# Kernel tuning notes

Measured on AMD Instinct MI355X. Metric: run time of the kernel, lower is better.

The kernel has to match this reference:

```python
import jax, jax.numpy as jnp
import numpy as np

TOPK = 8
NUM_SEM = 32


def _forward(x, sem_w, sem_b, q_w, k_w, v_w, fuse_w, fuse_b, alpha, ln_gamma, ln_beta):
    B, C, H, W = x.shape
    N = H * W
    xf = x.reshape(B, C, N)

    # semantic soft-assignment (softmax over K regions per position)
    sem_logits = jnp.einsum('kc,bcn->bkn', sem_w, xf) + sem_b[None, :, None]
    sem = jax.nn.softmax(sem_logits, axis=1)
    sem = jnp.nan_to_num(sem, posinf=1e-6, neginf=0.0)

    # 1x1 conv projections as GEMMs
    q = jnp.einsum('dc,bcn->bdn', q_w, xf)   # (B,d,N)
    k = jnp.einsum('dc,bcn->bdn', k_w, xf)   # (B,d,N)
    v = jnp.einsum('oc,bcn->bon', v_w, xf)   # (B,C,N)
    d = q.shape[1]
    scale = d ** 0.5 + 1e-6

    # --- dense semantic-region attention branch ---
    region_k = jnp.einsum('bkn,bdn->bkd', sem, k)
    region_v = jnp.einsum('bkn,bcn->bkc', sem, v)
    attn_region = jax.nn.softmax(jnp.einsum('bdn,bkd->bkn', q, region_k) / scale, axis=1)
    attn_region = jnp.nan_to_num(attn_region, posinf=1e6, neginf=-1e6)
    cont_out = jnp.einsum('bkn,bkc->bcn', attn_region, region_v)
    cont_out = jnp.nan_to_num(cont_out, posinf=1e6, neginf=-1e6)

    # --- sparse top-k gather attention branch ---
    M = min(256, N)
    _, ti = jax.lax.top_k(jax.lax.stop_gradient(sem), M)       # (B,K,M) top positions per region
    hr = jnp.argmax(sem, axis=1)                                # (B,N) hard region per position
    idx_pp = jnp.take_along_axis(ti, hr[:, :, None], axis=1)    # (B,N,M) pool indices for each position

    bidx = jnp.arange(B)[:, None, None]
    qt = jnp.swapaxes(q, 1, 2)  # (B,N,d)
    kt = jnp.swapaxes(k, 1, 2)  # (B,N,d)
    vt = jnp.swapaxes(v, 1, 2)  # (B,N,C)

    kg = kt[bidx, idx_pp]                                       # (B,N,M,d) gathered key pool
    sims = jnp.einsum('bnd,bnmd->bnm', qt, kg) / scale          # (B,N,M)
    kn = min(TOPK, M)
    topv, topi = jax.lax.top_k(sims, kn)                        # (B,N,kn)
    att = jax.nn.softmax(topv, axis=-1)
    actual = jnp.take_along_axis(idx_pp, topi, axis=2)          # (B,N,kn) spatial indices
    vg = vt[bidx, actual]                                       # (B,N,kn,C)
    sparse_out = jnp.swapaxes(jnp.einsum('bnt,bntc->bnc', att, vg), 1, 2)  # (B,C,N)
    sparse_out = jnp.nan_to_num(sparse_out, posinf=1e6, neginf=-1e6)

    # --- combine, fuse, residual, channel LayerNorm ---
    a = jax.nn.sigmoid(alpha)
    combined = a * cont_out + (1.0 - a) * sparse_out
    combined = jnp.nan_to_num(combined, posinf=1e6, neginf=-1e6)
    fused = jnp.einsum('oc,bcn->bon', fuse_w, combined) + fuse_b[None, :, None]
    out = x + fused.reshape(B, C, H, W)

    xp = out.transpose(0, 2, 3, 1)  # (B,H,W,C)
    mu = xp.mean(-1, keepdims=True)
    var = xp.var(-1, keepdims=True)
    xp = (xp - mu) / jnp.sqrt(var + 1e-5) * ln_gamma + ln_beta
    return xp.transpose(0, 3, 1, 2)


def setup_inputs() -> dict:
    key = jax.random.key(0)
    ks = jax.random.split(key, 8)
    B, C, H, W = 2, 256, 64, 64
    d = C // 4  # reduction=4
    Ksem = NUM_SEM
    f32 = jnp.float32
    return {
        'x': jax.random.normal(ks[0], (B, C, H, W), f32),
        'sem_w': jax.random.normal(ks[1], (Ksem, C), f32) * 0.05,
        'sem_b': jnp.zeros((Ksem,), f32),
        'q_w': jax.random.normal(ks[2], (d, C), f32) * (2.0 / C) ** 0.5,
        'k_w': jax.random.normal(ks[3], (d, C), f32) * (2.0 / C) ** 0.5,
        'v_w': jax.random.normal(ks[4], (C, C), f32) * (2.0 / C) ** 0.5,
        'fuse_w': jax.random.normal(ks[5], (C, C), f32) * (1.0 / C) ** 0.5,
        'fuse_b': jnp.zeros((C,), f32),
        'alpha': jnp.float32(0.5),
        'ln_gamma': jnp.ones((C,), f32),
        'ln_beta': jnp.zeros((C,), f32),
    }


def reference(x, sem_w, sem_b, q_w, k_w, v_w, fuse_w, fuse_b, alpha, ln_gamma, ln_beta):
    return _forward(x, sem_w, sem_b, q_w, k_w, v_w, fuse_w, fuse_b, alpha, ln_gamma, ln_beta)
```

## Files before the change

### kernel.cpp

```cpp
#include <hip/hip_runtime.h>
#include <math.h>

#define QOFF 32
#define KOFF 96
#define VOFF 160
#define NSUB 8

__global__ __launch_bounds__(256) void proj_kernel(
    const float* __restrict__ x,
    const float* __restrict__ sem_w, const float* __restrict__ sem_b,
    const float* __restrict__ q_w, const float* __restrict__ k_w,
    const float* __restrict__ v_w, float* __restrict__ Y)
{
    const int t = threadIdx.x;
    const int n0 = blockIdx.x * 64;
    const int oc0 = blockIdx.y * 64;
    const int b = blockIdx.z;
    const int ty = t >> 4, tx = t & 15;

    __shared__ float As[16][68];
    __shared__ float Bs[16][64];

    float acc[4][4];
#pragma unroll
    for (int i = 0; i < 4; i++)
#pragma unroll
        for (int j = 0; j < 4; j++) acc[i][j] = 0.f;

    const int oc_l = t >> 2;
    const int cp = t & 3;
    const int oc_g = oc0 + oc_l;
    const float* wrow = nullptr;
    if (oc_g < 32) wrow = sem_w + oc_g * 256;
    else if (oc_g < 96) wrow = q_w + (oc_g - 32) * 256;
    else if (oc_g < 160) wrow = k_w + (oc_g - 96) * 256;
    else if (oc_g < 416) wrow = v_w + (oc_g - 160) * 256;

    const int bk = t >> 4;
    const int bn = (t & 15) << 2;

    for (int c0 = 0; c0 < 256; c0 += 16) {
        __syncthreads();
        float4 w4 = make_float4(0.f, 0.f, 0.f, 0.f);
        if (wrow) w4 = *(const float4*)(wrow + c0 + (cp << 2));
        As[(cp << 2) + 0][oc_l] = w4.x;
        As[(cp << 2) + 1][oc_l] = w4.y;
        As[(cp << 2) + 2][oc_l] = w4.z;
        As[(cp << 2) + 3][oc_l] = w4.w;
        *(float4*)&Bs[bk][bn] =
            *(const float4*)(x + ((size_t)(b * 256 + c0 + bk)) * 4096 + n0 + bn);
        __syncthreads();
#pragma unroll
        for (int kk = 0; kk < 16; kk++) {
            float4 a4 = *(float4*)&As[kk][ty << 2];
            float4 b4 = *(float4*)&Bs[kk][tx << 2];
            acc[0][0] += a4.x * b4.x; acc[0][1] += a4.x * b4.y;
            acc[0][2] += a4.x * b4.z; acc[0][3] += a4.x * b4.w;
            acc[1][0] += a4.y * b4.x; acc[1][1] += a4.y * b4.y;
            acc[1][2] += a4.y * b4.z; acc[1][3] += a4.y * b4.w;
            acc[2][0] += a4.z * b4.x; acc[2][1] += a4.z * b4.y;
            acc[2][2] += a4.z * b4.z; acc[2][3] += a4.z * b4.w;
            acc[3][0] += a4.w * b4.x; acc[3][1] += a4.w * b4.y;
            acc[3][2] += a4.w * b4.z; acc[3][3] += a4.w * b4.w;
        }
    }

    if (oc0 + (ty << 2) < 416) {
        float bias[4];
#pragma unroll
        for (int i = 0; i < 4; i++) {
            int oc = oc0 + (ty << 2) + i;
            bias[i] = (oc < 32) ? sem_b[oc] : 0.f;
        }
#pragma unroll
        for (int j = 0; j < 4; j++) {
            int n = n0 + (tx << 2) + j;
            float4 o4 = make_float4(acc[0][j] + bias[0], acc[1][j] + bias[1],
                                    acc[2][j] + bias[2], acc[3][j] + bias[3]);
            *(float4*)(Y + ((size_t)(b * 4096 + n)) * 416 + oc0 + (ty << 2)) = o4;
        }
    }
}

__global__ __launch_bounds__(256) void semsoft_kernel(float* __restrict__ Y,
                                                      int* __restrict__ hr)
{
    const int g = blockIdx.x * 256 + threadIdx.x;
    float* row = Y + (size_t)g * 416;
    float v[32];
#pragma unroll
    for (int i = 0; i < 8; i++) *(float4*)&v[i * 4] = *(float4*)&row[i * 4];
    float mx = v[0]; int am = 0;
#pragma unroll
    for (int kk = 1; kk < 32; kk++) if (v[kk] > mx) { mx = v[kk]; am = kk; }
    float s = 0.f;
#pragma unroll
    for (int kk = 0; kk < 32; kk++) { v[kk] = expf(v[kk] - mx); s += v[kk]; }
    const float inv = 1.f / s;
#pragma unroll
    for (int kk = 0; kk < 32; kk++) v[kk] *= inv;
#pragma unroll
    for (int i = 0; i < 8; i++) *(float4*)&row[i * 4] = *(float4*)&v[i * 4];
    hr[g] = am;
}

__global__ __launch_bounds__(256) void bin_kernel(
    const int* __restrict__ hr, int* __restrict__ cnt, int* __restrict__ plist)
{
    const int g = blockIdx.x * 256 + threadIdx.x;
    const int b = g >> 12, n = g & 4095;
    const int r = hr[g];
    const int slot = atomicAdd(&cnt[b * 32 + r], 1);
    plist[((size_t)(b * 32 + r)) * 4096 + slot] = n;
}

__global__ __launch_bounds__(256) void region_partial_kernel(
    const float* __restrict__ Y, float* __restrict__ P)
{
    const int ch = blockIdx.x;
    const int b  = blockIdx.y;
    const int dg = blockIdx.z;
    const int t = threadIdx.x;
    __shared__ float sem_s[16][33];
    __shared__ float kv_s[16][68];
    const int kg = t >> 4;
    const int dq = t & 15;
    float acc[2][4];
#pragma unroll
    for (int i = 0; i < 2; i++)
#pragma unroll
        for (int j = 0; j < 4; j++) acc[i][j] = 0.f;

    const size_t gbase = (size_t)(b * 4096 + ch * 128);
    const int sr = t >> 4, sc = (t & 15) << 2;
    for (int r0 = 0; r0 < 128; r0 += 16) {
        __syncthreads();
        {
            sem_s[t >> 5][t & 31] = Y[(gbase + r0 + (t >> 5)) * 416 + (t & 31)];
            const int i2 = t + 256;
            sem_s[i2 >> 5][i2 & 31] = Y[(gbase + r0 + (i2 >> 5)) * 416 + (i2 & 31)];
        }
        {
            *(float4*)&kv_s[sr][sc] =
                *(const float4*)(Y + (gbase + r0 + sr) * 416 + 96 + dg * 64 + sc);
        }
        __syncthreads();
#pragma unroll
        for (int r = 0; r < 16; r++) {
            const float s0 = sem_s[r][(kg << 1) + 0];
            const float s1 = sem_s[r][(kg << 1) + 1];
            const float4 kv = *(float4*)&kv_s[r][dq << 2];
            acc[0][0] += s0 * kv.x; acc[0][1] += s0 * kv.y;
            acc[0][2] += s0 * kv.z; acc[0][3] += s0 * kv.w;
            acc[1][0] += s1 * kv.x; acc[1][1] += s1 * kv.y;
            acc[1][2] += s1 * kv.z; acc[1][3] += s1 * kv.w;
        }
    }
    float* Pb = P + ((size_t)(b * 32 + ch)) * 10240 + dg * 64;
#pragma unroll
    for (int i = 0; i < 2; i++)
        *(float4*)&Pb[((kg << 1) + i) * 320 + (dq << 2)] =
            make_float4(acc[i][0], acc[i][1], acc[i][2], acc[i][3]);
}

__global__ __launch_bounds__(256) void region_reduce_kernel(
    const float* __restrict__ P, float* __restrict__ region)
{
    const int idx = blockIdx.x * 256 + threadIdx.x;
    if (idx >= 2 * 10240) return;
    const int b = idx / 10240, rem = idx - b * 10240;
    float s = 0.f;
    for (int ch = 0; ch < 32; ch++)
        s += P[((size_t)(b * 32 + ch)) * 10240 + rem];
    region[(size_t)b * 10240 + rem] = s;
}

__global__ __launch_bounds__(256) void topk_sem_kernel(
    const float* __restrict__ Y, int* __restrict__ ti)
{
    const int kreg = blockIdx.x, b = blockIdx.y;
    const int t = threadIdx.x;
    __shared__ int wpart[4];
    __shared__ int sh_eq[256];
    __shared__ int ctr;

    unsigned int uv[16];
    const int nbase = t * 16;
#pragma unroll
    for (int i = 0; i < 16; i++) {
        float v = Y[((size_t)(b * 4096 + nbase + i)) * 416 + kreg];
        unsigned int u = __float_as_uint(v);
        uv[i] = (u & 0x80000000u) ? ~u : (u | 0x80000000u);
    }
    unsigned long long lo = 0ull, hi = 0xFFFFFFFFull;
    while (lo < hi) {
        const unsigned int mid = (unsigned int)((lo + hi + 1ull) >> 1);
        int c = 0;
#pragma unroll
        for (int i = 0; i < 16; i++) c += (uv[i] >= mid) ? 1 : 0;
#pragma unroll
        for (int off = 1; off < 64; off <<= 1) c += __shfl_xor(c, off);
        __syncthreads();
        if ((t & 63) == 0) wpart[t >> 6] = c;
        __syncthreads();
        const int tot = wpart[0] + wpart[1] + wpart[2] + wpart[3];
        if (tot >= 256) lo = mid; else hi = (unsigned long long)mid - 1ull;
    }
    const unsigned int T = (unsigned int)lo;
    int cgt = 0, ceq = 0;
#pragma unroll
    for (int i = 0; i < 16; i++) { cgt += (uv[i] > T) ? 1 : 0; ceq += (uv[i] == T) ? 1 : 0; }
    int cg = cgt;
#pragma unroll
    for (int off = 1; off < 64; off <<= 1) cg += __shfl_xor(cg, off);
    __syncthreads();
    if ((t & 63) == 0) wpart[t >> 6] = cg;
    sh_eq[t] = ceq;
    if (t == 0) ctr = 0;
    __syncthreads();
    const int c1 = wpart[0] + wpart[1] + wpart[2] + wpart[3];
    int eqbase = 0;
    for (int i = 0; i < t; i++) eqbase += sh_eq[i];
    int* outp = ti + ((size_t)(b * 32 + kreg)) * 256;
    int seen = 0;
#pragma unroll
    for (int i = 0; i < 16; i++) {
        if (uv[i] > T) {
            int pos = atomicAdd(&ctr, 1);
            outp[pos] = nbase + i;
        } else if (uv[i] == T) {
            int r = eqbase + seen; seen++;
            if (c1 + r < 256) outp[c1 + r] = nbase + i;
        }
    }
}

__global__ __launch_bounds__(256) void sparse_attn_kernel(
    const float* __restrict__ Y, const int* __restrict__ cnt,
    const int* __restrict__ plist, const int* __restrict__ ti,
    float* __restrict__ sp)
{
    const int rb = blockIdx.x;
    const int sub = blockIdx.y;
    const int b = rb >> 5;
    const int t = threadIdx.x, wid = t >> 6, lane = t & 63;

    int count = cnt[rb];
    count = min(max(count, 0), 4096);
    const int chunk = (count + NSUB - 1) / NSUB;
    const int p0 = sub * chunk;
    const int p1 = min(p0 + chunk, count);
    if (p1 <= p0) return;
    const int npass = (p1 - p0 + 15) >> 4;

    __shared__ int pool_s[256];
    __shared__ float K_sT[64][256];
    __shared__ float q_sT[4][64][4];

    if (t < 64)
        *(int4*)&pool_s[t << 2] = *(const int4*)(ti + (size_t)rb * 256 + (t << 2));
    __syncthreads();
    {
        const int krow = t >> 1, jh = t & 1;
#pragma unroll
        for (int hh = 0; hh < 2; hh++) {
            const int key = (hh << 7) + krow;
            const int kidx = pool_s[key];
            const float* kr = Y + ((size_t)((b << 12) + kidx)) * 416 + KOFF + (jh << 5);
#pragma unroll
            for (int jj = 0; jj < 8; jj++) {
                float4 kv = *(const float4*)(kr + (jj << 2));
                const int jb = (jh << 5) + (jj << 2);
                K_sT[jb + 0][key] = kv.x;
                K_sT[jb + 1][key] = kv.y;
                K_sT[jb + 2][key] = kv.z;
                K_sT[jb + 3][key] = kv.w;
            }
        }
    }
    __syncthreads();

    const float inv_scale = 1.0f / (8.0f + 1e-6f);
    const int* myplist = plist + (size_t)rb * 4096;

    for (int pass = 0; pass < npass; pass++) {
        int gg[4]; bool val[4];
#pragma unroll
        for (int p = 0; p < 4; p++) {
            const int idx = p0 + (pass << 4) + (wid << 2) + p;
            val[p] = (idx < p1);
            const int n = myplist[val[p] ? idx : p0];
            gg[p] = (b << 12) + n;
            q_sT[wid][lane][p] = Y[(size_t)gg[p] * 416 + QOFF + lane];
        }
        asm volatile("s_waitcnt lgkmcnt(0)" ::: "memory");

        float a[4][4];
#pragma unroll
        for (int p = 0; p < 4; p++)
#pragma unroll
            for (int sl = 0; sl < 4; sl++) a[p][sl] = 0.f;
#pragma unroll
        for (int j = 0; j < 64; j++) {
            const float2 k0 = *(const float2*)&K_sT[j][lane << 1];
            const float2 k1 = *(const float2*)&K_sT[j][128 + (lane << 1)];
            const float4 q4 = *(const float4*)&q_sT[wid][j][0];
            a[0][0] += q4.x * k0.x; a[0][1] += q4.x * k0.y;
            a[0][2] += q4.x * k1.x; a[0][3] += q4.x * k1.y;
            a[1][0] += q4.y * k0.x; a[1][1] += q4.y * k0.y;
            a[1][2] += q4.y * k1.x; a[1][3] += q4.y * k1.y;
            a[2][0] += q4.z * k0.x; a[2][1] += q4.z * k0.y;
            a[2][2] += q4.z * k1.x; a[2][3] += q4.z * k1.y;
            a[3][0] += q4.w * k0.x; a[3][1] += q4.w * k0.y;
            a[3][2] += q4.w * k1.x; a[3][3] += q4.w * k1.y;
        }

#pragma unroll
        for (int p = 0; p < 4; p++) {
            if (!val[p]) continue;
            float s0 = a[p][0] * inv_scale, s1 = a[p][1] * inv_scale;
            float s2 = a[p][2] * inv_scale, s3 = a[p][3] * inv_scale;
            const int m0 = lane << 1;
            float topv[8]; int topm[8];
#pragma unroll
            for (int sel = 0; sel < 8; sel++) {
                float bv = s0; int bm = m0;
                if (s1 > bv) { bv = s1; bm = m0 + 1; }
                if (s2 > bv) { bv = s2; bm = 128 + m0; }
                if (s3 > bv) { bv = s3; bm = 128 + m0 + 1; }
#pragma unroll
                for (int off = 1; off < 64; off <<= 1) {
                    const float ov = __shfl_xor(bv, off);
                    const int om = __shfl_xor(bm, off);
                    if (ov > bv || (ov == bv && om < bm)) { bv = ov; bm = om; }
                }
                topv[sel] = bv; topm[sel] = bm;
                const int owner = (bm & 127) >> 1;
                const int sl = (bm & 1) | ((bm >> 7) << 1);
                if (lane == owner) {
                    s0 = (sl == 0) ? -3e38f : s0;
                    s1 = (sl == 1) ? -3e38f : s1;
                    s2 = (sl == 2) ? -3e38f : s2;
                    s3 = (sl == 3) ? -3e38f : s3;
                }
            }
            const float mx = topv[0];
            float att[8]; float esum = 0.f;
#pragma unroll
            for (int j = 0; j < 8; j++) { att[j] = expf(topv[j] - mx); esum += att[j]; }
            const float inv = 1.f / esum;
            float4 acc = make_float4(0.f, 0.f, 0.f, 0.f);
#pragma unroll
            for (int j = 0; j < 8; j++) {
                const int actual = pool_s[topm[j]];
                const float4 vv = *(const float4*)(
                    Y + ((size_t)((b << 12) + actual)) * 416 + VOFF + (lane << 2));
                const float w = att[j] * inv;
                acc.x += w * vv.x; acc.y += w * vv.y;
                acc.z += w * vv.z; acc.w += w * vv.w;
            }
            *(float4*)(sp + (size_t)gg[p] * 256 + (lane << 2)) = acc;
        }
    }
}

__global__ __launch_bounds__(256) void combine_kernel(
    const float* __restrict__ Y, const float* __restrict__ region,
    const float* __restrict__ alpha, float* __restrict__ sp)
{
    const int t = threadIdx.x, wid = t >> 6, lane = t & 63;
    const int b = blockIdx.y;
    const int n0 = blockIdx.x << 5;
    __shared__ float rk_s[32][65];
    __shared__ float rv_s[32][256];
    __shared__ float q_all[32][64];

    const float* reg = region + (size_t)b * 10240;
    for (int idx = t; idx < 10240; idx += 256) {
        const int kk = idx / 320, dd = idx - kk * 320;
        const float v = reg[idx];
        if (dd < 64) rk_s[kk][dd] = v; else rv_s[kk][dd - 64] = v;
    }
    const size_t g0 = (size_t)(b << 12) + n0;
    for (int idx = t; idx < 2048; idx += 256)
        q_all[idx >> 6][idx & 63] = Y[(g0 + (idx >> 6)) * 416 + QOFF + (idx & 63)];
    __syncthreads();

    const float asig = 1.f / (1.f + expf(-alpha[0]));
    const float inv_scale = 1.0f / (8.0f + 1e-6f);
    const int kk = lane & 31, half = lane >> 5;

    for (int pp = 0; pp < 8; pp++) {
        const int n_l = (wid << 3) + pp;
        const size_t g = g0 + n_l;
        float part = 0.f;
        {
            const float* qr = &q_all[n_l][half << 5];
            const float* rkr = &rk_s[kk][half << 5];
#pragma unroll
            for (int j = 0; j < 32; j++) part += qr[j] * rkr[j];
        }
        part += __shfl_xor(part, 32);
        const float logit = part * inv_scale;
        float mx = logit;
#pragma unroll
        for (int off = 1; off < 32; off <<= 1) mx = fmaxf(mx, __shfl_xor(mx, off));
        const float e = expf(logit - mx);
        float s = e;
#pragma unroll
        for (int off = 1; off < 32; off <<= 1) s += __shfl_xor(s, off);
        const float w_own = e / s;

        float4 acc = make_float4(0.f, 0.f, 0.f, 0.f);
#pragma unroll
        for (int k2 = 0; k2 < 32; k2++) {
            const float w = __shfl(w_own, k2);
            const float4 rv = *(const float4*)&rv_s[k2][lane << 2];
            acc.x += w * rv.x; acc.y += w * rv.y;
            acc.z += w * rv.z; acc.w += w * rv.w;
        }
        float* spr = sp + g * 256 + (lane << 2);
        float4 spv = *(float4*)spr;
        float4 o;
        o.x = asig * acc.x + (1.f - asig) * spv.x;
        o.y = asig * acc.y + (1.f - asig) * spv.y;
        o.z = asig * acc.z + (1.f - asig) * spv.z;
        o.w = asig * acc.w + (1.f - asig) * spv.w;
        *(float4*)spr = o;
    }
}

__global__ __launch_bounds__(256) void fuse_ln_kernel(
    const float* __restrict__ comb, const float* __restrict__ fuse_w,
    const float* __restrict__ fuse_b, const float* __restrict__ x,
    const float* __restrict__ ln_g, const float* __restrict__ ln_b,
    float* __restrict__ out)
{
    const int t = threadIdx.x;
    const int n0 = blockIdx.x << 5;
    const int b = blockIdx.y;

    __shared__ float smem[32 * 256 + 32 * 36];
    float (*Ws)[256] = (float (*)[256])smem;
    float (*cs)[36] = (float (*)[36])(smem + 32 * 256);
    float (*Fs)[260] = (float (*)[260])smem;
    __shared__ float red1[8][32], red2[8][32];
    __shared__ float mu_s[32], rs_s[32];

    const int og = t & 63;
    const int ng = t >> 6;
    float acc[4][8];
#pragma unroll
    for (int i = 0; i < 4; i++)
#pragma unroll
        for (int j = 0; j < 8; j++) acc[i][j] = 0.f;

    const int cl = (t << 2) & 31;
    const int nl = t >> 3;

    for (int c0 = 0; c0 < 256; c0 += 32) {
        __syncthreads();
        {
            const float* wr = fuse_w + (size_t)t * 256 + c0;
#pragma unroll
            for (int j = 0; j < 8; j++) {
                float4 w4 = *(const float4*)(wr + (j << 2));
                Ws[(j << 2) + 0][t] = w4.x;
                Ws[(j << 2) + 1][t] = w4.y;
                Ws[(j << 2) + 2][t] = w4.z;
                Ws[(j << 2) + 3][t] = w4.w;
            }
        }
        {
            float4 c4 = *(const float4*)(
                comb + ((size_t)(b * 4096 + n0 + nl)) * 256 + c0 + cl);
            cs[cl + 0][nl] = c4.x;
            cs[cl + 1][nl] = c4.y;
            cs[cl + 2][nl] = c4.z;
            cs[cl + 3][nl] = c4.w;
        }
        __syncthreads();
#pragma unroll
        for (int cc = 0; cc < 32; cc++) {
            float4 w4 = *(float4*)&Ws[cc][og << 2];
            float4 ca = *(float4*)&cs[cc][ng << 3];
            float4 cb = *(float4*)&cs[cc][(ng << 3) + 4];
            float wv[4] = {w4.x, w4.y, w4.z, w4.w};
            float cv[8] = {ca.x, ca.y, ca.z, ca.w, cb.x, cb.y, cb.z, cb.w};
#pragma unroll
            for (int i = 0; i < 4; i++)
#pragma unroll
                for (int j = 0; j < 8; j++) acc[i][j] += wv[i] * cv[j];
        }
    }

    __syncthreads();
#pragma unroll
    for (int i = 0; i < 4; i++) {
        const int o = (og << 2) + i;
        const float fb = fuse_b[o];
        const float* xr = x + ((size_t)(b * 256 + o)) * 4096 + n0 + (ng << 3);
        float4 xa = *(const float4*)xr;
        float4 xb = *(const float4*)(xr + 4);
        float xv[8] = {xa.x, xa.y, xa.z, xa.w, xb.x, xb.y, xb.z, xb.w};
#pragma unroll
        for (int j = 0; j < 8; j++)
            Fs[(ng << 3) + j][o] = acc[i][j] + fb + xv[j];
    }
    __syncthreads();
    {
        const int n = t & 31, part = t >> 5;
        float s1 = 0.f, s2 = 0.f;
#pragma unroll
        for (int i = 0; i < 32; i++) {
            const float v = Fs[n][(part << 5) + i];
            s1 += v; s2 += v * v;
        }
        red1[part][n] = s1; red2[part][n] = s2;
    }
    __syncthreads();
    if (t < 32) {
        float s1 = 0.f, s2 = 0.f;
#pragma unroll
        for (int p = 0; p < 8; p++) { s1 += red1[p][t]; s2 += red2[p][t]; }
        const float mean = s1 * (1.f / 256.f);
        const float var = s2 * (1.f / 256.f) - mean * mean;
        mu_s[t] = mean;
        rs_s[t] = rsqrtf(var + 1e-5f);
    }
    __syncthreads();
#pragma unroll
    for (int j = 0; j < 32; j++) {
        const int idx = (j << 8) + t;
        const int o = idx >> 5, n = idx & 31;
        const float v = (Fs[n][o] - mu_s[n]) * rs_s[n] * ln_g[o] + ln_b[o];
        out[((size_t)(b * 256 + o)) * 4096 + n0 + n] = v;
    }
}

extern "C" void kernel_launch(void* const* d_in, const int* in_sizes, int n_in,
                              void* d_out, int out_size, void* d_ws, size_t ws_size,
                              hipStream_t stream)
{
    const float* x = (const float*)d_in[0];
    const float* sem_w = (const float*)d_in[1];
    const float* sem_b = (const float*)d_in[2];
    const float* q_w = (const float*)d_in[3];
    const float* k_w = (const float*)d_in[4];
    const float* v_w = (const float*)d_in[5];
    const float* fuse_w = (const float*)d_in[6];
    const float* fuse_b = (const float*)d_in[7];
    const float* alpha = (const float*)d_in[8];
    const float* ln_g = (const float*)d_in[9];
    const float* ln_b = (const float*)d_in[10];
    float* out = (float*)d_out;

    char* ws = (char*)d_ws;
    float* Y    = (float*)(ws);
    float* SP   = (float*)(ws + 13631488);
    float* P    = (float*)(ws + 22020096);
    float* REG  = (float*)(ws + 24641536);
    int*   HR   = (int*)  (ws + 24723456);
    int*   TI   = (int*)  (ws + 24756224);
    int*   CNT  = (int*)  (ws + 24821760);
    int*   PLIST= (int*)  (ws + 24822016);

    proj_kernel<<<dim3(64, 7, 2), 256, 0, stream>>>(x, sem_w, sem_b, q_w, k_w, v_w, Y);
    semsoft_kernel<<<32, 256, 0, stream>>>(Y, HR);
    hipMemsetAsync(CNT, 0, 256, stream);
    bin_kernel<<<32, 256, 0, stream>>>(HR, CNT, PLIST);
    region_partial_kernel<<<dim3(32, 2, 5), 256, 0, stream>>>(Y, P);
    region_reduce_kernel<<<80, 256, 0, stream>>>(P, REG);
    topk_sem_kernel<<<dim3(32, 2), 256, 0, stream>>>(Y, TI);
    sparse_attn_kernel<<<dim3(64, NSUB), 256, 0, stream>>>(Y, CNT, PLIST, TI, SP);
    combine_kernel<<<dim3(128, 2), 256, 0, stream>>>(Y, REG, alpha, SP);
    fuse_ln_kernel<<<dim3(128, 2), 256, 0, stream>>>(SP, fuse_w, fuse_b, x, ln_g, ln_b, out);
}
```

Measured before the change: 329.4 us.

## Replace iterative top-8 selection with bitonic merge of per-lane sorted lists

Rewrites the wavefront top-8 selection in the sparse attention kernel. Previously each of eight rounds did a full 6-step shuffle argmax reduction and then masked out the winner. Now each lane sorts its 4 candidates, and 6 butterfly steps each merge two sorted 8-lists with a bitonic half-cleaner plus sort. This cuts the serial dependency chain (8x6 rounds down to 6) at the cost of 16 shuffles per step and more registers, with the merge loop kept rolled.

New measurement: 472.1 us. 1.43x slower.

```diff
diff --git a/kernel.cpp b/kernel.cpp
--- a/kernel.cpp
+++ b/kernel.cpp
@@ -5,6 +5,14 @@
 #define KOFF 96
 #define VOFF 160
 #define NSUB 8
+
+#define GTPAIR(va,ia,vb,ib) (((va) > (vb)) || ((va) == (vb) && (ia) < (ib)))
+#define CE8(va,ia,vb,ib) { const bool c_ = GTPAIR(va,ia,vb,ib); \
+    const float hv_ = c_?(va):(vb), lv_ = c_?(vb):(va); \
+    const int   hi_ = c_?(ia):(ib), li_ = c_?(ib):(ia); \
+    (va)=hv_; (ia)=hi_; (vb)=lv_; (ib)=li_; }
+#define SELMAXP(wv,wi,va,ia,vb,ib) { const bool c_ = GTPAIR(va,ia,vb,ib); \
+    (wv) = c_?(va):(vb); (wi) = c_?(ia):(ib); }
 
 __global__ __launch_bounds__(256) void proj_kernel(
     const float* __restrict__ x,
@@ -318,46 +326,63 @@
 #pragma unroll
         for (int p = 0; p < 4; p++) {
             if (!val[p]) continue;
-            float s0 = a[p][0] * inv_scale, s1 = a[p][1] * inv_scale;
-            float s2 = a[p][2] * inv_scale, s3 = a[p][3] * inv_scale;
             const int m0 = lane << 1;
-            float topv[8]; int topm[8];
-#pragma unroll
-            for (int sel = 0; sel < 8; sel++) {
-                float bv = s0; int bm = m0;
-                if (s1 > bv) { bv = s1; bm = m0 + 1; }
-                if (s2 > bv) { bv = s2; bm = 128 + m0; }
-                if (s3 > bv) { bv = s3; bm = 128 + m0 + 1; }
-#pragma unroll
-                for (int off = 1; off < 64; off <<= 1) {
-                    const float ov = __shfl_xor(bv, off);
-                    const int om = __shfl_xor(bm, off);
-                    if (ov > bv || (ov == bv && om < bm)) { bv = ov; bm = om; }
+            float A0 = a[p][0] * inv_scale; int E0 = m0;
+            float A1 = a[p][1] * inv_scale; int E1 = m0 + 1;
+            float A2 = a[p][2] * inv_scale; int E2 = 128 + m0;
+            float A3 = a[p][3] * inv_scale; int E3 = 128 + m0 + 1;
+            CE8(A0,E0,A1,E1); CE8(A2,E2,A3,E3);
+            CE8(A0,E0,A2,E2); CE8(A1,E1,A3,E3); CE8(A1,E1,A2,E2);
+            float A4 = -3e38f, A5 = -3e38f, A6 = -3e38f, A7 = -3e38f;
+            int E4 = 2147483647, E5 = 2147483647, E6 = 2147483647, E7 = 2147483647;
+
+#pragma unroll 1
+            for (int off = 1; off < 64; off <<= 1) {
+                const float B0 = __shfl_xor(A0, off), B1 = __shfl_xor(A1, off);
+                const float B2 = __shfl_xor(A2, off), B3 = __shfl_xor(A3, off);
+                const float B4 = __shfl_xor(A4, off), B5 = __shfl_xor(A5, off);
+                const float B6 = __shfl_xor(A6, off), B7 = __shfl_xor(A7, off);
+                const int F0 = __shfl_xor(E0, off), F1 = __shfl_xor(E1, off);
+                const int F2 = __shfl_xor(E2, off), F3 = __shfl_xor(E3, off);
+                const int F4 = __shfl_xor(E4, off), F5 = __shfl_xor(E5, off);
+                const int F6 = __shfl_xor(E6, off), F7 = __shfl_xor(E7, off);
+                float W0,W1,W2,W3,W4,W5,W6,W7; int G0,G1,G2,G3,G4,G5,G6,G7;
+                SELMAXP(W0,G0, A0,E0, B7,F7);
+                SELMAXP(W1,G1, A1,E1, B6,F6);
+                SELMAXP(W2,G2, A2,E2, B5,F5);
+                SELMAXP(W3,G3, A3,E3, B4,F4);
+                SELMAXP(W4,G4, A4,E4, B3,F3);
+                SELMAXP(W5,G5, A5,E5, B2,F2);
+                SELMAXP(W6,G6, A6,E6, B1,F1);
+                SELMAXP(W7,G7, A7,E7, B0,F0);
+                CE8(W0,G0,W4,G4); CE8(W1,G1,W5,G5);
+                CE8(W2,G2,W6,G6); CE8(W3,G3,W7,G7);
+                CE8(W0,G0,W2,G2); CE8(W1,G1,W3,G3);
+                CE8(W4,G4,W6,G6); CE8(W5,G5,W7,G7);
+                CE8(W0,G0,W1,G1); CE8(W2,G2,W3,G3);
+                CE8(W4,G4,W5,G5); CE8(W6,G6,W7,G7);
+                A0=W0;E0=G0; A1=W1;E1=G1; A2=W2;E2=G2; A3=W3;E3=G3;
+                A4=W4;E4=G4; A5=W5;E5=G5; A6=W6;E6=G6; A7=W7;E7=G7;
+            }
+
+            const float w0 = 1.f,            w1 = expf(A1 - A0);
+            const float w2 = expf(A2 - A0), w3 = expf(A3 - A0);
+            const float w4 = expf(A4 - A0), w5 = expf(A5 - A0);
+            const float w6 = expf(A6 - A0), w7 = expf(A7 - A0);
+            const float inv = 1.f / (w0 + w1 + w2 + w3 + w4 + w5 + w6 + w7);
+            float4 acc = make_float4(0.f, 0.f, 0.f, 0.f);
+            {
+                const float ww[8] = {w0,w1,w2,w3,w4,w5,w6,w7};
+                const int   ee[8] = {E0,E1,E2,E3,E4,E5,E6,E7};
+#pragma unroll
+                for (int j = 0; j < 8; j++) {
+                    const int actual = pool_s[ee[j]];
+                    const float4 vv = *(const float4*)(
+                        Y + ((size_t)((b << 12) + actual)) * 416 + VOFF + (lane << 2));
+                    const float w = ww[j] * inv;
+                    acc.x += w * vv.x; acc.y += w * vv.y;
+                    acc.z += w * vv.z; acc.w += w * vv.w;
                 }
-                topv[sel] = bv; topm[sel] = bm;
-                const int owner = (bm & 127) >> 1;
-                const int sl = (bm & 1) | ((bm >> 7) << 1);
-                if (lane == owner) {
-                    s0 = (sl == 0) ? -3e38f : s0;
-                    s1 = (sl == 1) ? -3e38f : s1;
-                    s2 = (sl == 2) ? -3e38f : s2;
-                    s3 = (sl == 3) ? -3e38f : s3;
-                }
-            }
-            const float mx = topv[0];
-            float att[8]; float esum = 0.f;
-#pragma unroll
-            for (int j = 0; j < 8; j++) { att[j] = expf(topv[j] - mx); esum += att[j]; }
-            const float inv = 1.f / esum;
-            float4 acc = make_float4(0.f, 0.f, 0.f, 0.f);
-#pragma unroll
-            for (int j = 0; j < 8; j++) {
-                const int actual = pool_s[topm[j]];
-                const float4 vv = *(const float4*)(
-                    Y + ((size_t)((b << 12) + actual)) * 416 + VOFF + (lane << 2));
-                const float w = att[j] * inv;
-                acc.x += w * vv.x; acc.y += w * vv.y;
-                acc.z += w * vv.z; acc.w += w * vv.w;
             }
             *(float4*)(sp + (size_t)gg[p] * 256 + (lane << 2)) = acc;
         }
```
